# Kernel optimization log

Hardware: AMD Instinct MI355X
Metric: run time of the kernel (lower is better)

## Reference

```python
import jax, jax.numpy as jnp
import numpy as np

H, QK, VD = 16, 64, 64  # n_heads, qk_dim, v_dim

def _feature_map(t):
    # elu(x) + 1, the standard positive feature map for linear attention
    return jax.nn.elu(t) + 1.0

def setup_inputs() -> dict:
    key = jax.random.key(0)
    ks = jax.random.split(key, 5)
    B, T, D = 2, 4096, 1024
    s = 0.02
    return {
        "x": jax.random.normal(ks[0], (B, T, D), dtype=jnp.float32),
        "WQ": jax.random.normal(ks[1], (H * QK, D), dtype=jnp.float32) * s,
        "WK": jax.random.normal(ks[2], (H * QK, D), dtype=jnp.float32) * s,
        "WV": jax.random.normal(ks[3], (H * VD, D), dtype=jnp.float32) * s,
        "Wproj": jax.random.normal(ks[4], (D, VD), dtype=jnp.float32) * s,
        "start_pos": 0,
    }

def reference(x, WQ, WK, WV, Wproj, start_pos):
    B, T, D = x.shape
    # QKV projections (no bias), reshape to heads
    q = (x @ WQ.T).reshape(B, T, H, QK)
    k = (x @ WK.T).reshape(B, T, H, QK)
    v = (x @ WV.T).reshape(B, T, H, VD)
    q = _feature_map(q)
    k = _feature_map(k)
    # global key-value summary per head: [B,H,QK,VD]
    kv = jnp.einsum('bthd,bthm->bhdm', k, v)
    # normalizer: q . sum_t(k)
    z = 1.0 / jnp.einsum('bthd,bhd->bth', q, k.sum(axis=1))
    o = jnp.einsum('bthd,bhdm->bthm', q, kv) * z[..., None]  # [B,T,H,VD]
    # per-head output projection (module applies Linear(v_dim, dim) on last axis)
    return jnp.einsum('bthm,cm->bthc', o, Wproj)  # [B,T,H,D]
```

## Files before the change

### kernel.cpp

```cpp
#include <hip/hip_runtime.h>

#define Bb 2
#define Tt 4096
#define Dd 1024
#define Hh 16
#define QKd 64
#define VDd 64
#define BT (Bb*Tt)
#define NCH 8
#define CHUNK (Tt/NCH)

#define OFF_QF  0
#define OFF_KF  (OFF_QF + (size_t)BT*Dd)
#define OFF_V   (OFF_KF + (size_t)BT*512)
#define OFF_KVP (OFF_V + (size_t)BT*512)
#define OFF_KSP (OFF_KVP + (size_t)NCH*32*4096)
#define OFF_KV  (OFF_KSP + (size_t)NCH*32*64)
#define OFF_KS  (OFF_KV + (size_t)32*4096)
#define OFF_XA  (OFF_KS + (size_t)32*64)
#define OFF_WB  (OFF_XA + (size_t)BT*512)
#define OFF_KVQB (OFF_WB + (size_t)3072*512)
#define OFF_QSB (OFF_KVQB + (size_t)32*1024*32)

typedef __attribute__((ext_vector_type(8))) short short8;
typedef __attribute__((ext_vector_type(4))) float f32x4;

__device__ __forceinline__ float featmap(float x) {
    return x > 0.f ? x + 1.f : __expf(x);
}

__device__ __forceinline__ unsigned short bf16_rne(float f) {
    unsigned int u = __float_as_uint(f);
    unsigned int r = u + 0x7fffu + ((u >> 16) & 1u);
    return (unsigned short)(r >> 16);
}
__device__ __forceinline__ float bf16_to_f(unsigned short h) {
    return __uint_as_float(((unsigned int)h) << 16);
}

__global__ __launch_bounds__(256) void cast_all(const float* __restrict__ x,
                                                const float* __restrict__ WQ,
                                                const float* __restrict__ WK,
                                                const float* __restrict__ WV,
                                                unsigned short* __restrict__ xa,
                                                unsigned short* __restrict__ wbuf)
{
    int idx = blockIdx.x * 256 + threadIdx.x;
    if (idx < 2097152) {
        int m = idx >> 8;
        int c = (idx & 255) << 2;
        float4 v = *(const float4*)&x[(size_t)m * 1024 + c];
        ushort4 o;
        o.x = bf16_rne(v.x); o.y = bf16_rne(v.y); o.z = bf16_rne(v.z); o.w = bf16_rne(v.w);
        *(ushort4*)&xa[(size_t)m * 1024 + c] = o;
    } else {
        int r = idx - 2097152;
        int w = r >> 18;
        int rr = r & 262143;
        const float* src = (w == 0) ? WQ : ((w == 1) ? WK : WV);
        int m = rr >> 8;
        int c = (rr & 255) << 2;
        float4 v = *(const float4*)&src[(size_t)m * 1024 + c];
        ushort4 o;
        o.x = bf16_rne(v.x); o.y = bf16_rne(v.y); o.z = bf16_rne(v.z); o.w = bf16_rne(v.w);
        *(ushort4*)&wbuf[(size_t)(w*1024 + m) * 1024 + c] = o;
    }
}

#define GLLDS(gp, lp) __builtin_amdgcn_global_load_lds( \
    (const __attribute__((address_space(1))) void*)(gp), \
    (__attribute__((address_space(3))) void*)(lp), 16, 0, 0)

__global__ __launch_bounds__(512, 2) void gemm_qkv(const unsigned short* __restrict__ A,
                                                   const unsigned short* __restrict__ W,
                                                   float* __restrict__ qf,
                                                   unsigned short* __restrict__ kfb,
                                                   unsigned short* __restrict__ vfb)
{
    extern __shared__ unsigned short lds[];
    const int tid  = threadIdx.x;
    const int lane = tid & 63;
    const int wave = tid >> 6;
    const int wm = (wave >> 2) * 128;
    const int wn = (wave & 3) * 64;
    const int bid = blockIdx.x;
    const int nb = (bid & 7) * 48 + (bid >> 3);
    const int mblk = nb / 12, nblk = nb % 12;
    const int m0 = mblk * 256, n0 = nblk * 256;

    f32x4 acc[8][4] = {};

    auto stage = [&](int buf, int kt) {
        const int k0 = kt * 64;
        unsigned short* ab = &lds[buf * 32768];
        unsigned short* bb = ab + 16384;
        #pragma unroll
        for (int i = 0; i < 4; ++i) {
            int s = i * 512 + tid;
            int row = s >> 3, g = s & 7;
            int gl = g ^ (row & 7);
            GLLDS(&A[(size_t)(m0 + row) * 1024 + k0 + gl * 8], &ab[s * 8]);
        }
        #pragma unroll
        for (int i = 0; i < 4; ++i) {
            int s = i * 512 + tid;
            int row = s >> 3, g = s & 7;
            int gl = g ^ (row & 7);
            GLLDS(&W[(size_t)(n0 + row) * 1024 + k0 + gl * 8], &bb[s * 8]);
        }
    };

    stage(0, 0);
    for (int kt = 0; kt < 16; ++kt) {
        const int buf = kt & 1;
        if (kt + 1 < 16) {
            stage(buf ^ 1, kt + 1);
            asm volatile("s_waitcnt vmcnt(8)" ::: "memory");
        } else {
            asm volatile("s_waitcnt vmcnt(0)" ::: "memory");
        }
        __builtin_amdgcn_s_barrier();
        __builtin_amdgcn_sched_barrier(0);
        const unsigned short* ab = &lds[buf * 32768];
        const unsigned short* bb = ab + 16384;
        #pragma unroll
        for (int ks = 0; ks < 2; ++ks) {
            short8 af[8], bf2[4];
            #pragma unroll
            for (int mi = 0; mi < 8; ++mi) {
                int row = wm + mi * 16 + (lane & 15);
                int g = ks * 4 + (lane >> 4);
                af[mi] = *(const short8*)&ab[row * 64 + (g ^ (row & 7)) * 8];
            }
            #pragma unroll
            for (int ni = 0; ni < 4; ++ni) {
                int row = wn + ni * 16 + (lane & 15);
                int g = ks * 4 + (lane >> 4);
                bf2[ni] = *(const short8*)&bb[row * 64 + (g ^ (row & 7)) * 8];
            }
            __builtin_amdgcn_s_setprio(1);
            #pragma unroll
            for (int mi = 0; mi < 8; ++mi)
                #pragma unroll
                for (int ni = 0; ni < 4; ++ni)
                    acc[mi][ni] = __builtin_amdgcn_mfma_f32_16x16x32_bf16(af[mi], bf2[ni], acc[mi][ni], 0, 0, 0);
            __builtin_amdgcn_s_setprio(0);
        }
        __builtin_amdgcn_s_barrier();
        __builtin_amdgcn_sched_barrier(0);
    }

    const int c0 = n0 & 1023;
    if (n0 < 1024) {
        #pragma unroll
        for (int mi = 0; mi < 8; ++mi)
            #pragma unroll
            for (int ni = 0; ni < 4; ++ni)
                #pragma unroll
                for (int r = 0; r < 4; ++r) {
                    int row = m0 + wm + mi*16 + ((lane >> 4) << 2) + r;
                    int col = c0 + wn + ni*16 + (lane & 15);
                    qf[(size_t)row * 1024 + col] = featmap(acc[mi][ni][r]);
                }
    } else if (n0 < 2048) {
        #pragma unroll
        for (int mi = 0; mi < 8; ++mi)
            #pragma unroll
            for (int ni = 0; ni < 4; ++ni)
                #pragma unroll
                for (int r = 0; r < 4; ++r) {
                    int row = m0 + wm + mi*16 + ((lane >> 4) << 2) + r;
                    int col = c0 + wn + ni*16 + (lane & 15);
                    kfb[(size_t)row * 1024 + col] = bf16_rne(featmap(acc[mi][ni][r]));
                }
    } else {
        #pragma unroll
        for (int mi = 0; mi < 8; ++mi)
            #pragma unroll
            for (int ni = 0; ni < 4; ++ni)
                #pragma unroll
                for (int r = 0; r < 4; ++r) {
                    int row = m0 + wm + mi*16 + ((lane >> 4) << 2) + r;
                    int col = c0 + wn + ni*16 + (lane & 15);
                    vfb[(size_t)row * 1024 + col] = bf16_rne(acc[mi][ni][r]);
                }
    }
}

__global__ __launch_bounds__(256) void kv_partial(const unsigned short* __restrict__ kfb,
        const unsigned short* __restrict__ vfb, float* __restrict__ kvpart,
        float* __restrict__ kspart)
{
    const int bh = blockIdx.x;
    const int ch = blockIdx.y;
    const int b = bh >> 4, h = bh & 15;
    __shared__ float sk[32][68];
    __shared__ float sv[32][68];
    const int tid = threadIdx.x;
    const int r0 = (tid >> 4) << 2;
    const int c0 = (tid & 15) << 2;
    const int which = tid >> 7;
    const int rr = (tid & 127) >> 2;
    const int d16 = (tid & 3) << 4;
    const unsigned short* src = which ? vfb : kfb;
    float acc[4][4] = {};
    float ksl = 0.f;
    for (int t0 = ch * CHUNK; t0 < (ch + 1) * CHUNK; t0 += 32) {
        const int t = t0 + rr;
        const unsigned short* sp = &src[(size_t)(b*Tt + t)*Dd + h*QKd + d16];
        ushort4 ua = *(const ushort4*)&sp[0];
        ushort4 ub = *(const ushort4*)&sp[4];
        ushort4 uc = *(const ushort4*)&sp[8];
        ushort4 ud = *(const ushort4*)&sp[12];
        float4 f0 = {bf16_to_f(ua.x), bf16_to_f(ua.y), bf16_to_f(ua.z), bf16_to_f(ua.w)};
        float4 f1 = {bf16_to_f(ub.x), bf16_to_f(ub.y), bf16_to_f(ub.z), bf16_to_f(ub.w)};
        float4 f2 = {bf16_to_f(uc.x), bf16_to_f(uc.y), bf16_to_f(uc.z), bf16_to_f(uc.w)};
        float4 f3 = {bf16_to_f(ud.x), bf16_to_f(ud.y), bf16_to_f(ud.z), bf16_to_f(ud.w)};
        __syncthreads();
        float* dst = which ? &sv[rr][d16] : &sk[rr][d16];
        *(float4*)&dst[0]  = f0;
        *(float4*)&dst[4]  = f1;
        *(float4*)&dst[8]  = f2;
        *(float4*)&dst[12] = f3;
        __syncthreads();
        #pragma unroll 8
        for (int s = 0; s < 32; ++s) {
            float4 k4v = *(const float4*)&sk[s][r0];
            float4 v4v = *(const float4*)&sv[s][c0];
            float kvv[4] = {k4v.x,k4v.y,k4v.z,k4v.w};
            float vvv[4] = {v4v.x,v4v.y,v4v.z,v4v.w};
            #pragma unroll
            for (int i = 0; i < 4; ++i)
                #pragma unroll
                for (int j = 0; j < 4; ++j)
                    acc[i][j] = fmaf(kvv[i], vvv[j], acc[i][j]);
        }
        if (tid < 64) {
            #pragma unroll 8
            for (int s = 0; s < 32; ++s) ksl += sk[s][tid];
        }
    }
    const size_t base = (size_t)(ch*32 + bh) * 4096;
    #pragma unroll
    for (int i = 0; i < 4; ++i) {
        float4 o = {acc[i][0], acc[i][1], acc[i][2], acc[i][3]};
        *(float4*)&kvpart[base + (r0+i)*64 + c0] = o;
    }
    if (tid < 64) kspart[(size_t)(ch*32 + bh)*64 + tid] = ksl;
}

__global__ __launch_bounds__(256) void kv_reduce(const float* __restrict__ kvpart,
        const float* __restrict__ kspart, float* __restrict__ kv, float* __restrict__ ksum)
{
    int g = blockIdx.x * 256 + threadIdx.x;
    if (g < 32*4096) {
        float s = 0.f;
        #pragma unroll
        for (int c = 0; c < NCH; ++c) s += kvpart[(size_t)c*(32*4096) + g];
        kv[g] = s;
    } else if (g < 32*4096 + 32*64) {
        int g2 = g - 32*4096;
        float s = 0.f;
        #pragma unroll
        for (int c = 0; c < NCH; ++c) s += kspart[(size_t)c*(32*64) + g2];
        ksum[g2] = s;
    }
}

__global__ __launch_bounds__(256) void kvpb_kernel(const float* __restrict__ kv,
        const float* __restrict__ wproj, unsigned short* __restrict__ kvqb)
{
    int flat = blockIdx.x * 256 + threadIdx.x;
    int d = flat & 63;
    int c = (flat >> 6) & 1023;
    int bh = flat >> 16;
    const float4* kr = (const float4*)&kv[(size_t)(bh*64 + d)*64];
    const float4* wr = (const float4*)&wproj[(size_t)c*64];
    float s = 0.f;
    #pragma unroll
    for (int m = 0; m < 16; ++m) {
        float4 a = kr[m], bq = wr[m];
        s += a.x*bq.x + a.y*bq.y + a.z*bq.z + a.w*bq.w;
    }
    kvqb[((size_t)bh*1024 + c) * 64 + d] = bf16_rne(s);
}

__global__ __launch_bounds__(256) void zq_kernel(const float* __restrict__ qf,
        const float* __restrict__ ksum, unsigned short* __restrict__ qsb)
{
    int row = blockIdx.x * 16 + (threadIdx.x >> 4);
    int l16 = threadIdx.x & 15;
    int bt = row >> 4, h = row & 15;
    int b = bt >> 12, t = bt & 4095;
    float4 qv = *(const float4*)&qf[(size_t)bt*1024 + h*64 + l16*4];
    float4 kq = *(const float4*)&ksum[(size_t)(b*16 + h)*64 + l16*4];
    float p = qv.x*kq.x + qv.y*kq.y + qv.z*kq.z + qv.w*kq.w;
    p += __shfl_xor(p, 1); p += __shfl_xor(p, 2);
    p += __shfl_xor(p, 4); p += __shfl_xor(p, 8);
    float zv = 1.f / p;
    ushort4 o;
    o.x = bf16_rne(qv.x*zv); o.y = bf16_rne(qv.y*zv);
    o.z = bf16_rne(qv.z*zv); o.w = bf16_rne(qv.w*zv);
    *(ushort4*)&qsb[(((size_t)(b*16 + h)*4096 + t) << 6) + l16*4] = o;
}

__global__ __launch_bounds__(256) void fgemm(const unsigned short* __restrict__ qsb,
        const unsigned short* __restrict__ kvqb, float* __restrict__ out)
{
    __shared__ unsigned short Als[2][128*32];
    __shared__ unsigned short Bls[2][128*32];
    const int tid  = threadIdx.x;
    const int lane = tid & 63;
    const int wave = tid >> 6;
    const int bh = blockIdx.z;
    const int b = bh >> 4, h = bh & 15;
    const int t0 = blockIdx.y * 128;
    const int c0 = blockIdx.x * 128;
    const int wr = (wave >> 1) * 64;
    const int wc = (wave & 1) * 64;
    f32x4 acc[4][4] = {};

    auto stage = [&](int buf, int kt) {
        const int k0 = kt * 32;
        #pragma unroll
        for (int i = 0; i < 2; ++i) {
            int s = i * 256 + tid;
            int row = s >> 2, g = s & 3;
            GLLDS(&qsb[((size_t)bh*4096 + t0 + row) * 64 + k0 + g * 8], &Als[buf][s * 8]);
            GLLDS(&kvqb[((size_t)bh*1024 + c0 + row) * 64 + k0 + g * 8], &Bls[buf][s * 8]);
        }
    };

    stage(0, 0);
    const int arow = (lane & 15) * 32 + (lane >> 4) * 8;
    for (int kt = 0; kt < 2; ++kt) {
        const int buf = kt & 1;
        __syncthreads();
        if (kt + 1 < 2) stage(buf ^ 1, kt + 1);
        short8 af[4], bfr[4];
        #pragma unroll
        for (int m = 0; m < 4; ++m)
            af[m] = *(const short8*)&Als[buf][(wr + m*16)*32 + arow];
        #pragma unroll
        for (int n = 0; n < 4; ++n)
            bfr[n] = *(const short8*)&Bls[buf][(wc + n*16)*32 + arow];
        #pragma unroll
        for (int m = 0; m < 4; ++m)
            #pragma unroll
            for (int n = 0; n < 4; ++n)
                acc[m][n] = __builtin_amdgcn_mfma_f32_16x16x32_bf16(af[m], bfr[n], acc[m][n], 0, 0, 0);
    }

    #pragma unroll
    for (int m = 0; m < 4; ++m) {
        #pragma unroll
        for (int n = 0; n < 4; ++n) {
            #pragma unroll
            for (int r = 0; r < 4; ++r) {
                int trow = t0 + wr + m*16 + ((lane >> 4) << 2) + r;
                int col = c0 + wc + n*16 + (lane & 15);
                out[((size_t)(b*4096 + trow)*16 + h)*1024 + col] = acc[m][n][r];
            }
        }
    }
}

extern "C" void kernel_launch(void* const* d_in, const int* in_sizes, int n_in,
                              void* d_out, int out_size, void* d_ws, size_t ws_size,
                              hipStream_t stream)
{
    const float* x  = (const float*)d_in[0];
    const float* WQ = (const float*)d_in[1];
    const float* WK = (const float*)d_in[2];
    const float* WV = (const float*)d_in[3];
    const float* Wp = (const float*)d_in[4];
    float* ws = (float*)d_ws;
    float* qf     = ws + OFF_QF;
    unsigned short* kfb = (unsigned short*)(ws + OFF_KF);
    unsigned short* vfb = (unsigned short*)(ws + OFF_V);
    float* kvpart = ws + OFF_KVP;
    float* kspart = ws + OFF_KSP;
    float* kv     = ws + OFF_KV;
    float* ksum   = ws + OFF_KS;
    unsigned short* xa   = (unsigned short*)(ws + OFF_XA);
    unsigned short* wb   = (unsigned short*)(ws + OFF_WB);
    unsigned short* kvqb = (unsigned short*)(ws + OFF_KVQB);
    unsigned short* qsb  = (unsigned short*)(ws + OFF_QSB);
    float* out = (float*)d_out;

    (void)hipFuncSetAttribute((const void*)gemm_qkv,
                              hipFuncAttributeMaxDynamicSharedMemorySize, 131072);

    dim3 blk(256);
    cast_all<<<(2097152 + 786432)/256, blk, 0, stream>>>(x, WQ, WK, WV, xa, wb);
    gemm_qkv<<<384, 512, 131072, stream>>>(xa, wb, qf, kfb, vfb);
    kv_partial<<<dim3(32, NCH), blk, 0, stream>>>(kfb, vfb, kvpart, kspart);
    kv_reduce<<<(32*4096 + 32*64 + 255)/256, blk, 0, stream>>>(kvpart, kspart, kv, ksum);
    kvpb_kernel<<<(32*1024*64)/256, blk, 0, stream>>>(kv, Wp, kvqb);
    zq_kernel<<<(BT*Hh)/16, blk, 0, stream>>>(qf, ksum, qsb);
    fgemm<<<dim3(8, 32, 32), blk, 0, stream>>>(qsb, kvqb, out);
}
```

Before: 318.3 us.

## Keep Q tile resident and loop over output columns with double-buffered B staging

The final GEMM now assigns each block a 128-row Q tile for one (batch, head) and loops over all eight 128-column chunks of the projected KV matrix. The Q tile is loaded into LDS once, and the next B chunk is prefetched while the current one is computed and stored. This cuts grid size eightfold and removes redundant Q loads. The cost is fewer blocks and per-chunk barriers around the output stores. The kernel is dominated by writing a large fp32 output, so the gain is likely limited.

```diff
diff --git a/kernel.cpp b/kernel.cpp
--- a/kernel.cpp
+++ b/kernel.cpp
@@ -308,60 +308,80 @@
         const unsigned short* __restrict__ kvqb, float* __restrict__ out)
 {
     __shared__ unsigned short Als[2][128*32];
-    __shared__ unsigned short Bls[2][128*32];
+    __shared__ unsigned short Bls[2][2][128*32];
     const int tid  = threadIdx.x;
     const int lane = tid & 63;
     const int wave = tid >> 6;
-    const int bh = blockIdx.z;
+    const int bh = blockIdx.y;
     const int b = bh >> 4, h = bh & 15;
-    const int t0 = blockIdx.y * 128;
-    const int c0 = blockIdx.x * 128;
+    const int t0 = blockIdx.x * 128;
     const int wr = (wave >> 1) * 64;
     const int wc = (wave & 1) * 64;
-    f32x4 acc[4][4] = {};
-
-    auto stage = [&](int buf, int kt) {
-        const int k0 = kt * 32;
+
+    #pragma unroll
+    for (int kt = 0; kt < 2; ++kt)
         #pragma unroll
         for (int i = 0; i < 2; ++i) {
             int s = i * 256 + tid;
             int row = s >> 2, g = s & 3;
-            GLLDS(&qsb[((size_t)bh*4096 + t0 + row) * 64 + k0 + g * 8], &Als[buf][s * 8]);
-            GLLDS(&kvqb[((size_t)bh*1024 + c0 + row) * 64 + k0 + g * 8], &Bls[buf][s * 8]);
-        }
+            GLLDS(&qsb[((size_t)bh*4096 + t0 + row) * 64 + kt*32 + g * 8], &Als[kt][s * 8]);
+        }
+    auto stageB = [&](int buf, int c) {
+        #pragma unroll
+        for (int kt = 0; kt < 2; ++kt)
+            #pragma unroll
+            for (int i = 0; i < 2; ++i) {
+                int s = i * 256 + tid;
+                int row = s >> 2, g = s & 3;
+                GLLDS(&kvqb[((size_t)bh*1024 + c*128 + row) * 64 + kt*32 + g * 8],
+                      &Bls[buf][kt][s * 8]);
+            }
     };
-
-    stage(0, 0);
+    stageB(0, 0);
+
     const int arow = (lane & 15) * 32 + (lane >> 4) * 8;
-    for (int kt = 0; kt < 2; ++kt) {
-        const int buf = kt & 1;
-        __syncthreads();
-        if (kt + 1 < 2) stage(buf ^ 1, kt + 1);
-        short8 af[4], bfr[4];
-        #pragma unroll
-        for (int m = 0; m < 4; ++m)
-            af[m] = *(const short8*)&Als[buf][(wr + m*16)*32 + arow];
-        #pragma unroll
-        for (int n = 0; n < 4; ++n)
-            bfr[n] = *(const short8*)&Bls[buf][(wc + n*16)*32 + arow];
-        #pragma unroll
-        for (int m = 0; m < 4; ++m)
+    for (int c = 0; c < 8; ++c) {
+        const int buf = c & 1;
+        if (c + 1 < 8) {
+            stageB(buf ^ 1, c + 1);
+            asm volatile("s_waitcnt vmcnt(4)" ::: "memory");
+        } else {
+            asm volatile("s_waitcnt vmcnt(0)" ::: "memory");
+        }
+        __builtin_amdgcn_s_barrier();
+        __builtin_amdgcn_sched_barrier(0);
+
+        f32x4 acc[4][4] = {};
+        #pragma unroll
+        for (int kt = 0; kt < 2; ++kt) {
+            short8 af[4], bfr[4];
+            #pragma unroll
+            for (int m = 0; m < 4; ++m)
+                af[m] = *(const short8*)&Als[kt][(wr + m*16)*32 + arow];
             #pragma unroll
             for (int n = 0; n < 4; ++n)
-                acc[m][n] = __builtin_amdgcn_mfma_f32_16x16x32_bf16(af[m], bfr[n], acc[m][n], 0, 0, 0);
-    }
-
-    #pragma unroll
-    for (int m = 0; m < 4; ++m) {
-        #pragma unroll
-        for (int n = 0; n < 4; ++n) {
-            #pragma unroll
-            for (int r = 0; r < 4; ++r) {
-                int trow = t0 + wr + m*16 + ((lane >> 4) << 2) + r;
-                int col = c0 + wc + n*16 + (lane & 15);
-                out[((size_t)(b*4096 + trow)*16 + h)*1024 + col] = acc[m][n][r];
+                bfr[n] = *(const short8*)&Bls[buf][kt][(wc + n*16)*32 + arow];
+            #pragma unroll
+            for (int m = 0; m < 4; ++m)
+                #pragma unroll
+                for (int n = 0; n < 4; ++n)
+                    acc[m][n] = __builtin_amdgcn_mfma_f32_16x16x32_bf16(af[m], bfr[n], acc[m][n], 0, 0, 0);
+        }
+
+        #pragma unroll
+        for (int m = 0; m < 4; ++m) {
+            #pragma unroll
+            for (int n = 0; n < 4; ++n) {
+                #pragma unroll
+                for (int r = 0; r < 4; ++r) {
+                    int trow = t0 + wr + m*16 + ((lane >> 4) << 2) + r;
+                    int col = c*128 + wc + n*16 + (lane & 15);
+                    out[((size_t)(b*4096 + trow)*16 + h)*1024 + col] = acc[m][n][r];
+                }
             }
         }
+        __builtin_amdgcn_s_barrier();
+        __builtin_amdgcn_sched_barrier(0);
     }
 }
 
@@ -398,5 +418,5 @@
     kv_reduce<<<(32*4096 + 32*64 + 255)/256, blk, 0, stream>>>(kvpart, kspart, kv, ksum);
     kvpb_kernel<<<(32*1024*64)/256, blk, 0, stream>>>(kv, Wp, kvqb);
     zq_kernel<<<(BT*Hh)/16, blk, 0, stream>>>(qf, ksum, qsb);
-    fgemm<<<dim3(8, 32, 32), blk, 0, stream>>>(qsb, kvqb, out);
-}
+    fgemm<<<dim3(32, 32), blk, 0, stream>>>(qsb, kvqb, out);
+}
```

New measurement: 333.8 us. 1.05x slower.
